# Kernel optimization log

Measured on AMD Instinct MI355X. Metric: run time of the kernel, lower is better.

## Reference

```python
import jax, jax.numpy as jnp
import numpy as np

D_MODEL = 1024
N_HEADS = 16
D_K = D_MODEL // N_HEADS  # 64
D_V = D_MODEL // N_HEADS  # 64
BATCH = 2
SEQ = 2048


def setup_inputs() -> dict:
    key = jax.random.key(0)
    k_x, k_q, k_k, k_v, k_o = jax.random.split(key, 5)
    s = 1.0 / np.sqrt(D_MODEL)
    return {
        "X": jax.random.normal(k_x, (BATCH, SEQ, D_MODEL), dtype=jnp.float32),
        "W_Q": jax.random.normal(k_q, (D_MODEL, N_HEADS * D_K), dtype=jnp.float32) * s,
        "W_K": jax.random.normal(k_k, (D_MODEL, N_HEADS * D_K), dtype=jnp.float32) * s,
        "W_V": jax.random.normal(k_v, (D_MODEL, N_HEADS * D_V), dtype=jnp.float32) * s,
        "W_0": jax.random.normal(k_o, (N_HEADS * D_V, D_MODEL), dtype=jnp.float32) * s,
    }


def reference(X, W_Q, W_K, W_V, W_0):
    B, S, _ = X.shape
    # Project and split heads: [B, S, H, Dk]
    Q = (X @ W_Q).reshape(B, S, N_HEADS, D_K)
    K = (X @ W_K).reshape(B, S, N_HEADS, D_K)
    V = (X @ W_V).reshape(B, S, N_HEADS, D_V)
    # NOTE: original torch code scales by sqrt(K.shape[1]) == sqrt(seq_len),
    # not sqrt(d_k). Reproduce that exactly.
    scale = jnp.sqrt(jnp.asarray(S, dtype=X.dtype))
    scores = jnp.einsum("bqhd,bkhd->bhqk", Q, K) / scale  # [B, H, S, S]
    attn = jax.nn.softmax(scores, axis=-1)
    out = jnp.einsum("bhqk,bkhd->bqhd", attn, V)  # [B, S, H, Dv]
    return out.reshape(B, S, N_HEADS * D_V) @ W_0
```

## Files before the change

kernel.cpp:

```cpp
#include <hip/hip_runtime.h>

#define D_MODEL 1024
#define SEQ     2048
#define BATCH   2
#define NH      16

using u16 = unsigned short;
typedef __bf16 bf16x8 __attribute__((ext_vector_type(8)));
typedef float  f32x4  __attribute__((ext_vector_type(4)));

__device__ __forceinline__ u16 f2bf(float f){
  union { __bf16 h; u16 u; } v; v.h = (__bf16)f; return v.u;
}

__device__ __forceinline__ void gload_lds16(const void* g, void* l){
  __builtin_amdgcn_global_load_lds(
      (const __attribute__((address_space(1))) void*)g,
      (__attribute__((address_space(3))) void*)l, 16, 0, 0);
}

__global__ __launch_bounds__(256) void k_prep(
    const float* __restrict__ X, u16* __restrict__ Xb,
    const float* __restrict__ wq, const float* __restrict__ wk,
    const float* __restrict__ wv, const float* __restrict__ w0,
    u16* __restrict__ oq, u16* __restrict__ ok,
    u16* __restrict__ ov, u16* __restrict__ o0)
{
  const int t = threadIdx.x;
  if (blockIdx.x < 4096){
    int i = blockIdx.x*256 + t;
    float4 v = ((const float4*)X)[i];
    ushort4 o; o.x=f2bf(v.x); o.y=f2bf(v.y); o.z=f2bf(v.z); o.w=f2bf(v.w);
    ((ushort4*)Xb)[i] = o;
    return;
  }
  const int bid = blockIdx.x - 4096;
  const int z = bid >> 8, rem = bid & 255;
  const int nt = (rem & 15)*64, kt = (rem >> 4)*64;
  const float* W; u16* O;
  if      (z==0){W=wq;O=oq;}
  else if (z==1){W=wk;O=ok;}
  else if (z==2){W=wv;O=ov;}
  else          {W=w0;O=o0;}
  __shared__ float T[64][65];
  int r0 = t>>4, cb = (t&15)*4;
  #pragma unroll
  for (int j=0;j<4;++j){
    int r = r0 + j*16;
    float4 v = *(const float4*)(W + (size_t)(kt + r)*1024 + nt + cb);
    T[r][cb] = v.x; T[r][cb+1] = v.y; T[r][cb+2] = v.z; T[r][cb+3] = v.w;
  }
  __syncthreads();
  #pragma unroll
  for (int j=0;j<4;++j){
    int rn = r0 + j*16;
    ushort4 o;
    o.x = f2bf(T[cb  ][rn]); o.y = f2bf(T[cb+1][rn]);
    o.z = f2bf(T[cb+2][rn]); o.w = f2bf(T[cb+3][rn]);
    *(ushort4*)(O + (size_t)(nt + rn)*1024 + kt + cb) = o;
  }
}

__global__ __launch_bounds__(256) void k_gemm_qkv(
    const u16* __restrict__ A, const u16* __restrict__ Bt,
    u16* __restrict__ Ob, float scaleQ)
{
  const int K = 1024, N = 3072;
  const int nwg = gridDim.x * gridDim.y;
  const int f = blockIdx.y * gridDim.x + blockIdx.x;
  const int sw = (f & 7) * (nwg >> 3) + (f >> 3);
  const int bxs = sw % gridDim.x, bys = sw / gridDim.x;
  const int bm = bys*128, bn = bxs*128;
  const float scl = (bn < 1024) ? scaleQ : 1.0f;
  const int lane = threadIdx.x & 63, w = threadIdx.x >> 6;
  const int hi = lane >> 4, c = lane & 15;
  const int wr = w >> 1, wc = w & 1;

  __shared__ u16 As[2][128*32];
  __shared__ u16 Bs[2][128*32];

  const int i0 = 2*w, i1 = 2*w+1;
  const int rA0 = i0*16 + (lane>>2), rA1 = i1*16 + (lane>>2);
  const int cA  = (lane&3)*8;
  const u16* aS0 = A  + (size_t)(bm + rA0)*K + cA;
  const u16* aS1 = A  + (size_t)(bm + rA1)*K + cA;
  const u16* bS0 = Bt + (size_t)(bn + rA0)*K + cA;
  const u16* bS1 = Bt + (size_t)(bn + rA1)*K + cA;

  auto stage = [&](int buf, int kk){
    gload_lds16(aS0 + kk, As[buf] + i0*512);
    gload_lds16(aS1 + kk, As[buf] + i1*512);
    gload_lds16(bS0 + kk, Bs[buf] + i0*512);
    gload_lds16(bS1 + kk, Bs[buf] + i1*512);
  };

  f32x4 acc[4][4];
  #pragma unroll
  for (int mi=0;mi<4;++mi)
    #pragma unroll
    for (int ni=0;ni<4;++ni) acc[mi][ni] = (f32x4){0.f,0.f,0.f,0.f};

  stage(0, 0);
  __syncthreads();
  int cur = 0;
  for (int kk = 0; kk < K; kk += 32){
    if (kk + 32 < K) stage(cur^1, kk + 32);
    const u16* as = As[cur];
    const u16* bs = Bs[cur];
    bf16x8 af[4], bfr[4];
    #pragma unroll
    for (int mi=0;mi<4;++mi)
      af[mi] = *(const bf16x8*)(as + (wr*64 + mi*16 + c)*32 + hi*8);
    #pragma unroll
    for (int ni=0;ni<4;++ni)
      bfr[ni] = *(const bf16x8*)(bs + (wc*64 + ni*16 + c)*32 + hi*8);
    #pragma unroll
    for (int mi=0;mi<4;++mi)
      #pragma unroll
      for (int ni=0;ni<4;++ni)
        acc[mi][ni] = __builtin_amdgcn_mfma_f32_16x16x32_bf16(af[mi], bfr[ni], acc[mi][ni], 0, 0, 0);
    __syncthreads();
    cur ^= 1;
  }
  #pragma unroll
  for (int mi=0;mi<4;++mi){
    #pragma unroll
    for (int ni=0;ni<4;++ni){
      int row = bm + wr*64 + mi*16 + hi*4;
      int col = bn + wc*64 + ni*16 + c;
      #pragma unroll
      for (int r=0;r<4;++r)
        Ob[(size_t)(row + r)*N + col] = f2bf(acc[mi][ni][r] * scl);
    }
  }
}

__global__ __launch_bounds__(256) void k_gemm_out(
    const u16* __restrict__ A, const u16* __restrict__ Bt,
    float* __restrict__ OF)
{
  const int K = 1024, N = 1024;
  const int nwg = gridDim.x * gridDim.y;
  const int f = blockIdx.y * gridDim.x + blockIdx.x;
  const int sw = (f & 7) * (nwg >> 3) + (f >> 3);
  const int bxs = sw % gridDim.x, bys = sw / gridDim.x;
  const int bm = bys*128, bn = bxs*128;
  const int lane = threadIdx.x & 63, w = threadIdx.x >> 6;
  const int hi = lane >> 4, c = lane & 15;
  const int wr = w >> 1, wc = w & 1;

  __shared__ u16 As[2][128*32];
  __shared__ u16 Bs[2][128*32];

  const int i0 = 2*w, i1 = 2*w+1;
  const int rA0 = i0*16 + (lane>>2), rA1 = i1*16 + (lane>>2);
  const int cA  = (lane&3)*8;
  const u16* aS0 = A  + (size_t)(bm + rA0)*K + cA;
  const u16* aS1 = A  + (size_t)(bm + rA1)*K + cA;
  const u16* bS0 = Bt + (size_t)(bn + rA0)*K + cA;
  const u16* bS1 = Bt + (size_t)(bn + rA1)*K + cA;

  auto stage = [&](int buf, int kk){
    gload_lds16(aS0 + kk, As[buf] + i0*512);
    gload_lds16(aS1 + kk, As[buf] + i1*512);
    gload_lds16(bS0 + kk, Bs[buf] + i0*512);
    gload_lds16(bS1 + kk, Bs[buf] + i1*512);
  };

  f32x4 acc[4][4];
  #pragma unroll
  for (int mi=0;mi<4;++mi)
    #pragma unroll
    for (int ni=0;ni<4;++ni) acc[mi][ni] = (f32x4){0.f,0.f,0.f,0.f};

  stage(0, 0);
  __syncthreads();
  int cur = 0;
  for (int kk = 0; kk < K; kk += 32){
    if (kk + 32 < K) stage(cur^1, kk + 32);
    const u16* as = As[cur];
    const u16* bs = Bs[cur];
    bf16x8 af[4], bfr[4];
    #pragma unroll
    for (int mi=0;mi<4;++mi)
      af[mi] = *(const bf16x8*)(as + (wr*64 + mi*16 + c)*32 + hi*8);
    #pragma unroll
    for (int ni=0;ni<4;++ni)
      bfr[ni] = *(const bf16x8*)(bs + (wc*64 + ni*16 + c)*32 + hi*8);
    #pragma unroll
    for (int mi=0;mi<4;++mi)
      #pragma unroll
      for (int ni=0;ni<4;++ni)
        acc[mi][ni] = __builtin_amdgcn_mfma_f32_16x16x32_bf16(af[mi], bfr[ni], acc[mi][ni], 0, 0, 0);
    __syncthreads();
    cur ^= 1;
  }
  #pragma unroll
  for (int mi=0;mi<4;++mi){
    #pragma unroll
    for (int ni=0;ni<4;++ni){
      int row = bm + wr*64 + mi*16 + hi*4;
      int col = bn + wc*64 + ni*16 + c;
      #pragma unroll
      for (int r=0;r<4;++r)
        OF[(size_t)(row + r)*N + col] = acc[mi][ni][r];
    }
  }
}

__global__ __launch_bounds__(256) void k_trans_v(const u16* __restrict__ QKV,
                                                 u16* __restrict__ Vt){
  int st = blockIdx.x, bh = blockIdx.y;
  int b = bh >> 4, h = bh & 15;
  __shared__ u16 T[64][80];
  int t = threadIdx.x;
  {
    int s = t >> 2, dc = (t & 3)*16;
    const u16* src = QKV + (size_t)(b*SEQ + st*64 + s)*3072 + 2048 + h*64 + dc;
    *(uint4*)&T[s][dc]   = *(const uint4*)(src);
    *(uint4*)&T[s][dc+8] = *(const uint4*)(src + 8);
  }
  __syncthreads();
  {
    int d = t >> 2, sc = (t & 3)*16;
    u16* dst = Vt + ((size_t)bh*64 + d)*SEQ + st*64 + sc;
    u16 vals[16];
    #pragma unroll
    for (int x=0;x<16;++x){
      int p = sc + x;
      int s = (p & 0x23) | ((p & 0x04) << 2) | ((p & 0x18) >> 1);
      vals[x] = T[s][d];
    }
    uint4 w0, w1;
    w0.x = (unsigned)vals[ 0] | ((unsigned)vals[ 1] << 16);
    w0.y = (unsigned)vals[ 2] | ((unsigned)vals[ 3] << 16);
    w0.z = (unsigned)vals[ 4] | ((unsigned)vals[ 5] << 16);
    w0.w = (unsigned)vals[ 6] | ((unsigned)vals[ 7] << 16);
    w1.x = (unsigned)vals[ 8] | ((unsigned)vals[ 9] << 16);
    w1.y = (unsigned)vals[10] | ((unsigned)vals[11] << 16);
    w1.z = (unsigned)vals[12] | ((unsigned)vals[13] << 16);
    w1.w = (unsigned)vals[14] | ((unsigned)vals[15] << 16);
    *(uint4*)(dst)     = w0;
    *(uint4*)(dst + 8) = w1;
  }
}

__global__ __launch_bounds__(256, 2) void k_attn(const u16* __restrict__ QKV,
                                                 const u16* __restrict__ Vt,
                                                 u16* __restrict__ AO)
{
  const int bh = blockIdx.x, qt = blockIdx.y;
  const int b = bh >> 4, h = bh & 15;
  const int lane = threadIdx.x & 63, w = threadIdx.x >> 6;
  const int qg = w >> 1, kh = w & 1;
  const int hi = lane >> 4, c = lane & 15;

  __shared__ u16 Ks[2][64*64];
  __shared__ u16 Vs[2][64*64];

  const size_t qrow0 = (size_t)(b*SEQ + qt*128 + qg*64 + c);
  bf16x8 qf0[4], qf1[4];
  #pragma unroll
  for (int s=0;s<4;++s){
    qf0[s] = *(const bf16x8*)(QKV + (qrow0 + s*16)*3072 + h*64 + hi*8);
    qf1[s] = *(const bf16x8*)(QKV + (qrow0 + s*16)*3072 + h*64 + 32 + hi*8);
  }

  bf16x8 ones8;
  #pragma unroll
  for (int j=0;j<8;++j) ones8[j] = (__bf16)1.0f;

  f32x4 acc_o[4][4];
  f32x4 acc_l[4];
  #pragma unroll
  for (int s=0;s<4;++s){
    acc_l[s] = (f32x4){0.f,0.f,0.f,0.f};
    #pragma unroll
    for (int n=0;n<4;++n) acc_o[s][n] = (f32x4){0.f,0.f,0.f,0.f};
  }

  const int r0 = w*8 + (lane>>3);
  const int r1 = 32 + r0;
  const int sb = ((((lane&7)*16) ^ ((lane>>3)<<4)) >> 1);
  const u16* kS0 = QKV + (size_t)(b*SEQ + r0)*3072 + 1024 + h*64 + sb;
  const u16* kS1 = QKV + (size_t)(b*SEQ + r1)*3072 + 1024 + h*64 + sb;
  const u16* vS0 = Vt + ((size_t)bh*64 + r0)*SEQ + sb;
  const u16* vS1 = Vt + ((size_t)bh*64 + r1)*SEQ + sb;

  auto stage = [&](int buf){
    gload_lds16(kS0, Ks[buf] + w*512);
    gload_lds16(kS1, Ks[buf] + 2048 + w*512);
    gload_lds16(vS0, Vs[buf] + w*512);
    gload_lds16(vS1, Vs[buf] + 2048 + w*512);
    kS0 += (size_t)64*3072; kS1 += (size_t)64*3072; vS0 += 64; vS1 += 64;
  };

  const int swz = ((c&7)<<4);
  const char* kr0 = (const char*)&Ks[0][0] + (kh*32 + c)*128 + (( 0 + hi*16) ^ swz);
  const char* kr1 = (const char*)&Ks[0][0] + (kh*32 + c)*128 + ((64 + hi*16) ^ swz);
  const char* vr  = (const char*)&Vs[0][0] + c*128 + ((kh*64 + hi*16) ^ swz);

  auto body = [&](int buf){
    const int bo = buf*8192;
    bf16x8 k00 = *(const bf16x8*)(kr0 + bo);
    bf16x8 k01 = *(const bf16x8*)(kr1 + bo);
    bf16x8 k10 = *(const bf16x8*)(kr0 + bo + 2048);
    bf16x8 k11 = *(const bf16x8*)(kr1 + bo + 2048);
    bf16x8 vv0 = *(const bf16x8*)(vr + bo);
    bf16x8 vv1 = *(const bf16x8*)(vr + bo + 2048);
    bf16x8 vv2 = *(const bf16x8*)(vr + bo + 4096);
    bf16x8 vv3 = *(const bf16x8*)(vr + bo + 6144);
    #pragma unroll
    for (int s=0;s<4;++s){
      f32x4 s0 = (f32x4){0.f,0.f,0.f,0.f};
      f32x4 s1 = (f32x4){0.f,0.f,0.f,0.f};
      __builtin_amdgcn_s_setprio(1);
      s0 = __builtin_amdgcn_mfma_f32_16x16x32_bf16(k00, qf0[s], s0, 0,0,0);
      s1 = __builtin_amdgcn_mfma_f32_16x16x32_bf16(k10, qf0[s], s1, 0,0,0);
      s0 = __builtin_amdgcn_mfma_f32_16x16x32_bf16(k01, qf1[s], s0, 0,0,0);
      s1 = __builtin_amdgcn_mfma_f32_16x16x32_bf16(k11, qf1[s], s1, 0,0,0);
      __builtin_amdgcn_s_setprio(0);
      bf16x8 a;
      #pragma unroll
      for (int i=0;i<4;++i){
        a[i]   = (__bf16)__builtin_amdgcn_exp2f(s0[i]);
        a[i+4] = (__bf16)__builtin_amdgcn_exp2f(s1[i]);
      }
      __builtin_amdgcn_s_setprio(1);
      acc_l[s]    = __builtin_amdgcn_mfma_f32_16x16x32_bf16(a, ones8, acc_l[s], 0,0,0);
      acc_o[s][0] = __builtin_amdgcn_mfma_f32_16x16x32_bf16(a, vv0, acc_o[s][0], 0,0,0);
      acc_o[s][1] = __builtin_amdgcn_mfma_f32_16x16x32_bf16(a, vv1, acc_o[s][1], 0,0,0);
      acc_o[s][2] = __builtin_amdgcn_mfma_f32_16x16x32_bf16(a, vv2, acc_o[s][2], 0,0,0);
      acc_o[s][3] = __builtin_amdgcn_mfma_f32_16x16x32_bf16(a, vv3, acc_o[s][3], 0,0,0);
      __builtin_amdgcn_s_setprio(0);
    }
  };

  stage(0);
  __syncthreads();
  #pragma unroll 1
  for (int u = 0; u < SEQ/128; ++u){
    stage(1);
    body(0);
    __syncthreads();
    if (u != SEQ/128 - 1) stage(0);
    body(1);
    __syncthreads();
  }

  float* Of = (float*)&Ks[0][0];
  float* Lf = (float*)&Vs[0][0];
  #pragma unroll
  for (int s=0;s<4;++s){
    if (kh == 1){
      #pragma unroll
      for (int n=0;n<4;++n)
        #pragma unroll
        for (int i=0;i<4;++i)
          Of[qg*1024 + (hi*4+i)*64 + n*16 + c] = acc_o[s][n][i];
      if (c == 0){
        #pragma unroll
        for (int i=0;i<4;++i) Lf[qg*16 + hi*4 + i] = acc_l[s][i];
      }
    }
    __syncthreads();
    if (kh == 0){
      float inv[4];
      #pragma unroll
      for (int i=0;i<4;++i)
        inv[i] = 1.0f / (acc_l[s][i] + Lf[qg*16 + hi*4 + i]);
      size_t obase = (size_t)(b*SEQ + qt*128 + qg*64 + s*16 + hi*4)*D_MODEL + h*64;
      #pragma unroll
      for (int i=0;i<4;++i){
        #pragma unroll
        for (int n=0;n<4;++n){
          float o = acc_o[s][n][i] + Of[qg*1024 + (hi*4+i)*64 + n*16 + c];
          AO[obase + (size_t)i*D_MODEL + n*16 + c] = f2bf(o * inv[i]);
        }
      }
    }
    __syncthreads();
  }
}

extern "C" void kernel_launch(void* const* d_in, const int* in_sizes, int n_in,
                              void* d_out, int out_size, void* d_ws, size_t ws_size,
                              hipStream_t stream)
{
  const float* X  = (const float*)d_in[0];
  const float* Wq = (const float*)d_in[1];
  const float* Wk = (const float*)d_in[2];
  const float* Wv = (const float*)d_in[3];
  const float* W0 = (const float*)d_in[4];
  float* out = (float*)d_out;

  char* ws = (char*)d_ws;
  const size_t MB = 1024*1024;
  u16* Xb    = (u16*)(ws);
  u16* WqkvT = (u16*)(ws +  8*MB);
  u16* W0T   = (u16*)(ws + 14*MB);
  u16* QKVb  = (u16*)(ws + 16*MB);
  u16* Vt    = (u16*)(ws + 40*MB);
  u16* AO    = Xb;

  const float scaleQ = 1.4426950408889634f / sqrtf((float)SEQ);
  const int M = BATCH*SEQ;

  k_prep<<<dim3(4096 + 1024), 256, 0, stream>>>(
      X, Xb, Wq, Wk, Wv, W0,
      WqkvT, WqkvT + 1024*1024, WqkvT + 2*1024*1024, W0T);
  k_gemm_qkv<<<dim3(3072/128, M/128), 256, 0, stream>>>(Xb, WqkvT, QKVb, scaleQ);
  k_trans_v<<<dim3(SEQ/64, BATCH*NH), 256, 0, stream>>>(QKVb, Vt);
  k_attn<<<dim3(BATCH*NH, SEQ/128), 256, 0, stream>>>(QKVb, Vt, AO);
  k_gemm_out<<<dim3(1024/128, M/128), 256, 0, stream>>>(AO, W0T, out);
}
```

Before: 107.2 us.

## Merge projection GEMMs into a templated kernel with 4-stage LDS pipeline

Replaces the two double-buffered projection GEMM kernels with one templated kernel that uses a four-deep LDS ring, prefetching three k-steps ahead with direct global-to-LDS loads. Each k-step is split into two MFMA phases interleaved with B-fragment reads and staged loads, with explicit vmcnt waits, barriers and s_setprio raised around the MFMA blocks. The aim is to hide global-load latency and keep the matrix units busy. It doubles LDS use per block (64 KB) while asking for two blocks per CU, and it adds more barriers per iteration.

```diff
diff --git a/kernel.cpp b/kernel.cpp
--- a/kernel.cpp
+++ b/kernel.cpp
@@ -61,38 +61,42 @@
   }
 }
 
-__global__ __launch_bounds__(256) void k_gemm_qkv(
+template<int MODE>
+__global__ __launch_bounds__(256, 2) void k_gemm_p(
     const u16* __restrict__ A, const u16* __restrict__ Bt,
-    u16* __restrict__ Ob, float scaleQ)
+    u16* __restrict__ Ob, float* __restrict__ OF, float scaleQ, int N)
 {
-  const int K = 1024, N = 3072;
+  const int K = 1024;
   const int nwg = gridDim.x * gridDim.y;
   const int f = blockIdx.y * gridDim.x + blockIdx.x;
   const int sw = (f & 7) * (nwg >> 3) + (f >> 3);
   const int bxs = sw % gridDim.x, bys = sw / gridDim.x;
   const int bm = bys*128, bn = bxs*128;
-  const float scl = (bn < 1024) ? scaleQ : 1.0f;
+  const float scl = (MODE == 0 && bn < 1024) ? scaleQ : 1.0f;
   const int lane = threadIdx.x & 63, w = threadIdx.x >> 6;
   const int hi = lane >> 4, c = lane & 15;
   const int wr = w >> 1, wc = w & 1;
-
-  __shared__ u16 As[2][128*32];
-  __shared__ u16 Bs[2][128*32];
-
-  const int i0 = 2*w, i1 = 2*w+1;
-  const int rA0 = i0*16 + (lane>>2), rA1 = i1*16 + (lane>>2);
-  const int cA  = (lane&3)*8;
-  const u16* aS0 = A  + (size_t)(bm + rA0)*K + cA;
-  const u16* aS1 = A  + (size_t)(bm + rA1)*K + cA;
-  const u16* bS0 = Bt + (size_t)(bn + rA0)*K + cA;
-  const u16* bS1 = Bt + (size_t)(bn + rA1)*K + cA;
-
-  auto stage = [&](int buf, int kk){
-    gload_lds16(aS0 + kk, As[buf] + i0*512);
-    gload_lds16(aS1 + kk, As[buf] + i1*512);
-    gload_lds16(bS0 + kk, Bs[buf] + i0*512);
-    gload_lds16(bS1 + kk, Bs[buf] + i1*512);
+  const int t = threadIdx.x;
+
+  __shared__ u16 As[4][128*32];
+  __shared__ u16 Bs[4][128*32];
+
+  const int sr = t >> 2, scol = (t & 3)*8;
+  const u16* aS0 = A  + (size_t)(bm + sr)*K + scol;
+  const u16* aS1 = A  + (size_t)(bm + 64 + sr)*K + scol;
+  const u16* bS0 = Bt + (size_t)(bn + sr)*K + scol;
+  const u16* bS1 = Bt + (size_t)(bn + 64 + sr)*K + scol;
+
+  auto stageA = [&](int v){
+    char* dst = (char*)&As[v & 3][0] + w*1024;
+    gload_lds16(aS0 + v*32, dst);
+    gload_lds16(aS1 + v*32, dst + 4096);
   };
+  auto stageB = [&](int v){
+    char* dst = (char*)&Bs[v & 3][0] + w*1024;
+    gload_lds16(bS0 + v*32, dst);
+    gload_lds16(bS1 + v*32, dst + 4096);
+  };
 
   f32x4 acc[4][4];
   #pragma unroll
@@ -100,28 +104,51 @@
     #pragma unroll
     for (int ni=0;ni<4;++ni) acc[mi][ni] = (f32x4){0.f,0.f,0.f,0.f};
 
-  stage(0, 0);
-  __syncthreads();
-  int cur = 0;
-  for (int kk = 0; kk < K; kk += 32){
-    if (kk + 32 < K) stage(cur^1, kk + 32);
-    const u16* as = As[cur];
-    const u16* bs = Bs[cur];
-    bf16x8 af[4], bfr[4];
+  stageA(0); stageB(0); stageA(1); stageB(1); stageA(2); stageB(2);
+  asm volatile("s_waitcnt vmcnt(8)" ::: "memory");
+  __builtin_amdgcn_sched_barrier(0);
+  __builtin_amdgcn_s_barrier();
+
+  #pragma unroll 1
+  for (int u = 0; u < 32; ++u){
+    const u16* as = &As[0][0] + (u & 3)*4096;
+    const u16* bs = &Bs[0][0] + (u & 3)*4096;
+    bf16x8 af[4];
     #pragma unroll
     for (int mi=0;mi<4;++mi)
       af[mi] = *(const bf16x8*)(as + (wr*64 + mi*16 + c)*32 + hi*8);
-    #pragma unroll
-    for (int ni=0;ni<4;++ni)
-      bfr[ni] = *(const bf16x8*)(bs + (wc*64 + ni*16 + c)*32 + hi*8);
-    #pragma unroll
-    for (int mi=0;mi<4;++mi)
-      #pragma unroll
-      for (int ni=0;ni<4;++ni)
-        acc[mi][ni] = __builtin_amdgcn_mfma_f32_16x16x32_bf16(af[mi], bfr[ni], acc[mi][ni], 0, 0, 0);
-    __syncthreads();
-    cur ^= 1;
-  }
+    bf16x8 bf0 = *(const bf16x8*)(bs + (wc*64 +  0 + c)*32 + hi*8);
+    bf16x8 bf1 = *(const bf16x8*)(bs + (wc*64 + 16 + c)*32 + hi*8);
+    if (u < 29) stageA(u+3);
+    __builtin_amdgcn_s_barrier();
+    __builtin_amdgcn_s_setprio(1);
+    #pragma unroll
+    for (int mi=0;mi<4;++mi){
+      acc[mi][0] = __builtin_amdgcn_mfma_f32_16x16x32_bf16(af[mi], bf0, acc[mi][0], 0,0,0);
+      acc[mi][1] = __builtin_amdgcn_mfma_f32_16x16x32_bf16(af[mi], bf1, acc[mi][1], 0,0,0);
+    }
+    __builtin_amdgcn_s_setprio(0);
+    __builtin_amdgcn_s_barrier();
+    bf16x8 bf2 = *(const bf16x8*)(bs + (wc*64 + 32 + c)*32 + hi*8);
+    bf16x8 bf3 = *(const bf16x8*)(bs + (wc*64 + 48 + c)*32 + hi*8);
+    if (u < 29) stageB(u+3);
+    if (u < 29){
+      asm volatile("s_waitcnt vmcnt(8)" ::: "memory");
+    } else if (u < 31){
+      asm volatile("s_waitcnt vmcnt(0)" ::: "memory");
+    }
+    __builtin_amdgcn_sched_barrier(0);
+    __builtin_amdgcn_s_barrier();
+    __builtin_amdgcn_s_setprio(1);
+    #pragma unroll
+    for (int mi=0;mi<4;++mi){
+      acc[mi][2] = __builtin_amdgcn_mfma_f32_16x16x32_bf16(af[mi], bf2, acc[mi][2], 0,0,0);
+      acc[mi][3] = __builtin_amdgcn_mfma_f32_16x16x32_bf16(af[mi], bf3, acc[mi][3], 0,0,0);
+    }
+    __builtin_amdgcn_s_setprio(0);
+    __builtin_amdgcn_s_barrier();
+  }
+
   #pragma unroll
   for (int mi=0;mi<4;++mi){
     #pragma unroll
@@ -129,81 +156,10 @@
       int row = bm + wr*64 + mi*16 + hi*4;
       int col = bn + wc*64 + ni*16 + c;
       #pragma unroll
-      for (int r=0;r<4;++r)
-        Ob[(size_t)(row + r)*N + col] = f2bf(acc[mi][ni][r] * scl);
-    }
-  }
-}
-
-__global__ __launch_bounds__(256) void k_gemm_out(
-    const u16* __restrict__ A, const u16* __restrict__ Bt,
-    float* __restrict__ OF)
-{
-  const int K = 1024, N = 1024;
-  const int nwg = gridDim.x * gridDim.y;
-  const int f = blockIdx.y * gridDim.x + blockIdx.x;
-  const int sw = (f & 7) * (nwg >> 3) + (f >> 3);
-  const int bxs = sw % gridDim.x, bys = sw / gridDim.x;
-  const int bm = bys*128, bn = bxs*128;
-  const int lane = threadIdx.x & 63, w = threadIdx.x >> 6;
-  const int hi = lane >> 4, c = lane & 15;
-  const int wr = w >> 1, wc = w & 1;
-
-  __shared__ u16 As[2][128*32];
-  __shared__ u16 Bs[2][128*32];
-
-  const int i0 = 2*w, i1 = 2*w+1;
-  const int rA0 = i0*16 + (lane>>2), rA1 = i1*16 + (lane>>2);
-  const int cA  = (lane&3)*8;
-  const u16* aS0 = A  + (size_t)(bm + rA0)*K + cA;
-  const u16* aS1 = A  + (size_t)(bm + rA1)*K + cA;
-  const u16* bS0 = Bt + (size_t)(bn + rA0)*K + cA;
-  const u16* bS1 = Bt + (size_t)(bn + rA1)*K + cA;
-
-  auto stage = [&](int buf, int kk){
-    gload_lds16(aS0 + kk, As[buf] + i0*512);
-    gload_lds16(aS1 + kk, As[buf] + i1*512);
-    gload_lds16(bS0 + kk, Bs[buf] + i0*512);
-    gload_lds16(bS1 + kk, Bs[buf] + i1*512);
-  };
-
-  f32x4 acc[4][4];
-  #pragma unroll
-  for (int mi=0;mi<4;++mi)
-    #pragma unroll
-    for (int ni=0;ni<4;++ni) acc[mi][ni] = (f32x4){0.f,0.f,0.f,0.f};
-
-  stage(0, 0);
-  __syncthreads();
-  int cur = 0;
-  for (int kk = 0; kk < K; kk += 32){
-    if (kk + 32 < K) stage(cur^1, kk + 32);
-    const u16* as = As[cur];
-    const u16* bs = Bs[cur];
-    bf16x8 af[4], bfr[4];
-    #pragma unroll
-    for (int mi=0;mi<4;++mi)
-      af[mi] = *(const bf16x8*)(as + (wr*64 + mi*16 + c)*32 + hi*8);
-    #pragma unroll
-    for (int ni=0;ni<4;++ni)
-      bfr[ni] = *(const bf16x8*)(bs + (wc*64 + ni*16 + c)*32 + hi*8);
-    #pragma unroll
-    for (int mi=0;mi<4;++mi)
-      #pragma unroll
-      for (int ni=0;ni<4;++ni)
-        acc[mi][ni] = __builtin_amdgcn_mfma_f32_16x16x32_bf16(af[mi], bfr[ni], acc[mi][ni], 0, 0, 0);
-    __syncthreads();
-    cur ^= 1;
-  }
-  #pragma unroll
-  for (int mi=0;mi<4;++mi){
-    #pragma unroll
-    for (int ni=0;ni<4;++ni){
-      int row = bm + wr*64 + mi*16 + hi*4;
-      int col = bn + wc*64 + ni*16 + c;
-      #pragma unroll
-      for (int r=0;r<4;++r)
-        OF[(size_t)(row + r)*N + col] = acc[mi][ni][r];
+      for (int r=0;r<4;++r){
+        if (MODE == 0) Ob[(size_t)(row + r)*N + col] = f2bf(acc[mi][ni][r] * scl);
+        else           OF[(size_t)(row + r)*N + col] = acc[mi][ni][r];
+      }
     }
   }
 }
@@ -409,8 +365,10 @@
   k_prep<<<dim3(4096 + 1024), 256, 0, stream>>>(
       X, Xb, Wq, Wk, Wv, W0,
       WqkvT, WqkvT + 1024*1024, WqkvT + 2*1024*1024, W0T);
-  k_gemm_qkv<<<dim3(3072/128, M/128), 256, 0, stream>>>(Xb, WqkvT, QKVb, scaleQ);
+  k_gemm_p<0><<<dim3(3072/128, M/128), 256, 0, stream>>>(
+      Xb, WqkvT, QKVb, nullptr, scaleQ, 3072);
   k_trans_v<<<dim3(SEQ/64, BATCH*NH), 256, 0, stream>>>(QKVb, Vt);
   k_attn<<<dim3(BATCH*NH, SEQ/128), 256, 0, stream>>>(QKVb, Vt, AO);
-  k_gemm_out<<<dim3(1024/128, M/128), 256, 0, stream>>>(AO, W0T, out);
-}
+  k_gemm_p<1><<<dim3(1024/128, M/128), 256, 0, stream>>>(
+      AO, W0T, nullptr, out, 1.0f, 1024);
+}
```

Measured after the change: 113.9 us. 1.06x slower.
